# Kernel tuning notes

Measured on AMD Instinct MI355X. Metric: run time of the kernel, lower is better.

The kernel has to match this reference:

```python
import jax, jax.numpy as jnp
import numpy as np
import math

B, S, H = 2, 4096, 768
NH, HD = 12, 64  # num heads, head dim


def setup_inputs() -> dict:
    key = jax.random.key(0)
    ks = jax.random.split(key, 4)
    scale = 1.0 / math.sqrt(H)
    return {
        "hidden_states": jax.random.normal(ks[0], (B, S, H), jnp.float32),
        "attention_mask": jnp.zeros((B, 1, 1, S), jnp.float32),
        "Wq": jax.random.normal(ks[1], (H, H), jnp.float32) * scale,
        "bq": jnp.zeros((H,), jnp.float32),
        "Wk": jax.random.normal(ks[2], (H, H), jnp.float32) * scale,
        "bk": jnp.zeros((H,), jnp.float32),
        "Wv": jax.random.normal(ks[3], (H, H), jnp.float32) * scale,
        "bv": jnp.zeros((H,), jnp.float32),
    }


def reference(hidden_states, attention_mask, Wq, bq, Wk, bk, Wv, bv):
    # Linear projections (torch nn.Linear: x @ W.T + b)
    q = hidden_states @ Wq.T + bq  # [B,S,H]
    k = hidden_states @ Wk.T + bk
    v = hidden_states @ Wv.T + bv
    # split heads -> [B, NH, S, HD]
    def split(x):
        return x.reshape(B, S, NH, HD).transpose(0, 2, 1, 3)
    qh, kh, vh = split(q), split(k), split(v)
    scores = jnp.einsum('bhqd,bhkd->bhqk', qh, kh) / math.sqrt(HD)
    scores = scores + attention_mask  # additive mask, broadcast
    probs = jax.nn.softmax(scores, axis=-1)
    # dropout prob = 0.0 (inference) -> identity
    ctx = jnp.einsum('bhqk,bhkd->bhqd', probs, vh)
    ctx = ctx.transpose(0, 2, 1, 3).reshape(B, S, H)
    return ctx
```

## Files before the change

### kernel.cpp

```cpp
#include <hip/hip_runtime.h>
#include <hip/hip_bf16.h>

typedef float f32x4 __attribute__((ext_vector_type(4)));
typedef short short8 __attribute__((ext_vector_type(8)));

#define LOG2E 1.44269504088896340736f

__device__ __forceinline__ ushort f2bf(float f){
  unsigned u = __builtin_bit_cast(unsigned, f);
  u = (u + 0x7fffu + ((u >> 16) & 1u)) >> 16;
  return (ushort)u;
}

__device__ __forceinline__ float exp2_hw(float x){
  float r; asm("v_exp_f32 %0, %1" : "=v"(r) : "v"(x)); return r;
}

__device__ __forceinline__ uint pack_bf16_rh(float lo, float hi){
  uint ul = __builtin_bit_cast(uint, lo) + 0x8000u;
  uint uh = __builtin_bit_cast(uint, hi) + 0x8000u;
  return __builtin_amdgcn_perm(uh, ul, 0x07060302u);
}

__device__ __forceinline__ float fmax3(float a, float b, float c){
  return fmaxf(fmaxf(a, b), c);
}

__global__ void cvt_kernel(const float* __restrict__ src, ushort* __restrict__ dst, int n4){
  int i = blockIdx.x * 256 + threadIdx.x;
  if (i < n4){
    float4 v = ((const float4*)src)[i];
    ushort4 o; o.x = f2bf(v.x); o.y = f2bf(v.y); o.z = f2bf(v.z); o.w = f2bf(v.w);
    ((ushort4*)dst)[i] = o;
  }
}

__global__ void scale_kernel(const float* __restrict__ src, float* __restrict__ dst,
                             float sc, int n){
  int i = blockIdx.x * 256 + threadIdx.x;
  if (i < n) dst[i] = src[i] * sc;
}

__global__ __launch_bounds__(256) void qkv_gemm(const ushort* __restrict__ Xb,
                                                const ushort* __restrict__ Wb,
                                                const float* __restrict__ bias,
                                                ushort* __restrict__ Out,
                                                float scale){
  __shared__ ushort Xs[128*64];
  __shared__ ushort Ws[128*64];
  const int m0 = blockIdx.x * 128, n0 = blockIdx.y * 128;
  const int tid = threadIdx.x, w = tid >> 6, lane = tid & 63;
  const int r = lane & 15, g = lane >> 4;
  const int wr = (w >> 1) * 64, wc = (w & 1) * 64;
  f32x4 acc[4][4] = {};
  for (int k0 = 0; k0 < 768; k0 += 64){
    #pragma unroll
    for (int p = 0; p < 4; p++){
      int c = tid + 256*p; int row = c >> 3, cir = c & 7;
      uint4 vx = *(const uint4*)(Xb + (size_t)(m0+row)*768 + k0 + cir*8);
      *(uint4*)((char*)Xs + row*128 + ((cir*16) ^ ((row&7)<<4))) = vx;
      uint4 vw = *(const uint4*)(Wb + (size_t)(n0+row)*768 + k0 + cir*8);
      *(uint4*)((char*)Ws + row*128 + ((cir*16) ^ ((row&7)<<4))) = vw;
    }
    __syncthreads();
    #pragma unroll
    for (int ks = 0; ks < 2; ks++){
      short8 af[4], bf[4];
      int bo = ks*64 + g*16;
      #pragma unroll
      for (int i = 0; i < 4; i++){
        int rowa = wr + i*16 + r;
        af[i] = *(const short8*)((char*)Xs + rowa*128 + (bo ^ ((rowa&7)<<4)));
        int rowb = wc + i*16 + r;
        bf[i] = *(const short8*)((char*)Ws + rowb*128 + (bo ^ ((rowb&7)<<4)));
      }
      #pragma unroll
      for (int i = 0; i < 4; i++)
        #pragma unroll
        for (int j = 0; j < 4; j++)
          acc[i][j] = __builtin_amdgcn_mfma_f32_16x16x32_bf16(af[i], bf[j], acc[i][j], 0,0,0);
    }
    __syncthreads();
  }
  #pragma unroll
  for (int i = 0; i < 4; i++){
    #pragma unroll
    for (int j = 0; j < 4; j++){
      int col = n0 + wc + j*16 + r;
      float bv = bias[col];
      int rowb = m0 + wr + i*16 + g*4;
      #pragma unroll
      for (int q = 0; q < 4; q++)
        Out[(size_t)(rowb+q)*768 + col] = f2bf((acc[i][j][q] + bv) * scale);
    }
  }
}

__global__ __launch_bounds__(256) void qkv_gemm_vt(const ushort* __restrict__ Xb,
                                                   const ushort* __restrict__ Wb,
                                                   const float* __restrict__ bias,
                                                   ushort* __restrict__ VtOut){
  __shared__ ushort Xs[128*64];
  __shared__ ushort Ws[128*64];
  const int m0 = blockIdx.x * 128, n0 = blockIdx.y * 128;
  const int tid = threadIdx.x, w = tid >> 6, lane = tid & 63;
  const int r = lane & 15, g = lane >> 4;
  const int wr = (w >> 1) * 64, wc = (w & 1) * 64;
  f32x4 acc[4][4] = {};
  for (int k0 = 0; k0 < 768; k0 += 64){
    #pragma unroll
    for (int p = 0; p < 4; p++){
      int c = tid + 256*p; int row = c >> 3, cir = c & 7;
      uint4 vx = *(const uint4*)(Xb + (size_t)(m0+row)*768 + k0 + cir*8);
      *(uint4*)((char*)Xs + row*128 + ((cir*16) ^ ((row&7)<<4))) = vx;
      uint4 vw = *(const uint4*)(Wb + (size_t)(n0+row)*768 + k0 + cir*8);
      *(uint4*)((char*)Ws + row*128 + ((cir*16) ^ ((row&7)<<4))) = vw;
    }
    __syncthreads();
    #pragma unroll
    for (int ks = 0; ks < 2; ks++){
      short8 af[4], bf[4];
      int bo = ks*64 + g*16;
      #pragma unroll
      for (int i = 0; i < 4; i++){
        int rowa = wr + i*16 + r;
        af[i] = *(const short8*)((char*)Xs + rowa*128 + (bo ^ ((rowa&7)<<4)));
        int rowb = wc + i*16 + r;
        bf[i] = *(const short8*)((char*)Ws + rowb*128 + (bo ^ ((rowb&7)<<4)));
      }
      #pragma unroll
      for (int i = 0; i < 4; i++)
        #pragma unroll
        for (int j = 0; j < 4; j++)
          acc[i][j] = __builtin_amdgcn_mfma_f32_16x16x32_bf16(af[i], bf[j], acc[i][j], 0,0,0);
    }
    __syncthreads();
  }
  #pragma unroll
  for (int i = 0; i < 4; i++){
    #pragma unroll
    for (int j = 0; j < 4; j++){
      int col = n0 + wc + j*16 + r;
      float bv = bias[col];
      int rowb = m0 + wr + i*16 + g*4;
      ushort4 o;
      o.x = f2bf(acc[i][j][0] + bv);
      o.y = f2bf(acc[i][j][1] + bv);
      o.z = f2bf(acc[i][j][2] + bv);
      o.w = f2bf(acc[i][j][3] + bv);
      size_t vrow = (size_t)((rowb >> 12) * 768 + col);
      *(ushort4*)(VtOut + vrow * 4096 + (rowb & 4095)) = o;
    }
  }
}

__global__ __launch_bounds__(256, 3) void flash_attn(const ushort* __restrict__ Qb,
                                                     const ushort* __restrict__ Kb,
                                                     const ushort* __restrict__ Vt,
                                                     const float* __restrict__ maskL,
                                                     float* __restrict__ out){
  __shared__ ushort Ks[64*64];
  __shared__ ushort Vts[64*64];
  __shared__ ushort Ps[4][2048];
  const int tid = threadIdx.x, w = tid >> 6, lane = tid & 63;
  const int r = lane & 15, g = lane >> 4;
  const int swr = (r & 7) << 4;
  const int h = blockIdx.y, b = blockIdx.z;
  const int q0 = blockIdx.x * 128 + w * 32;
  char* Pw = (char*)(Ps[w]);

  short8 bq[2][2];
  #pragma unroll
  for (int grp = 0; grp < 2; grp++){
    const ushort* qp = Qb + (size_t)(b*4096 + q0 + grp*16 + r)*768 + h*64 + g*8;
    bq[grp][0] = *(const short8*)qp;
    bq[grp][1] = *(const short8*)(qp + 32);
  }
  const ushort* Kbase = Kb + (size_t)(b*4096)*768 + h*64;
  const ushort* Vbase = Vt + (size_t)(b*768 + h*64)*4096;

  const int row0 = tid >> 3, cir = tid & 7;
  const int row1 = row0 + 32;

  uint4 kreg0, kreg1, vreg0, vreg1;
  kreg0 = *(const uint4*)(Kbase + (size_t)row0*768 + cir*8);
  kreg1 = *(const uint4*)(Kbase + (size_t)row1*768 + cir*8);
  vreg0 = *(const uint4*)(Vbase + (size_t)row0*4096 + cir*8);
  vreg1 = *(const uint4*)(Vbase + (size_t)row1*4096 + cir*8);

  f32x4 ctx[2][4] = {};
  float mrun[2] = {-1e30f, -1e30f}, lrun[2] = {0.f, 0.f};

  for (int t = 0; t < 64; t++){
    const int kv0 = t * 64;
    *(uint4*)((char*)Ks  + row0*128 + ((cir*16) ^ ((row0&7)<<4))) = kreg0;
    *(uint4*)((char*)Ks  + row1*128 + ((cir*16) ^ ((row1&7)<<4))) = kreg1;
    *(uint4*)((char*)Vts + row0*128 + ((cir*16) ^ ((row0&7)<<4))) = vreg0;
    *(uint4*)((char*)Vts + row1*128 + ((cir*16) ^ ((row1&7)<<4))) = vreg1;
    __syncthreads();
    if (t < 63){
      const int kn = kv0 + 64;
      kreg0 = *(const uint4*)(Kbase + (size_t)(kn+row0)*768 + cir*8);
      kreg1 = *(const uint4*)(Kbase + (size_t)(kn+row1)*768 + cir*8);
      vreg0 = *(const uint4*)(Vbase + (size_t)row0*4096 + kn + cir*8);
      vreg1 = *(const uint4*)(Vbase + (size_t)row1*4096 + kn + cir*8);
    }
    f32x4 s[2][4];
    #pragma unroll
    for (int c = 0; c < 4; c++){
      int row = c*16 + r; int sw = (row&7) << 4;
      const char* base = (const char*)Ks + row*128;
      short8 ak0 = *(const short8*)(base + ((g*16) ^ sw));
      short8 ak1 = *(const short8*)(base + ((64 + g*16) ^ sw));
      #pragma unroll
      for (int grp = 0; grp < 2; grp++){
        f32x4 z = {};
        z = __builtin_amdgcn_mfma_f32_16x16x32_bf16(ak0, bq[grp][0], z, 0,0,0);
        z = __builtin_amdgcn_mfma_f32_16x16x32_bf16(ak1, bq[grp][1], z, 0,0,0);
        s[grp][c] = z;
      }
    }
    #pragma unroll
    for (int c = 0; c < 4; c++){
      float4 mv = *(const float4*)(maskL + b*4096 + kv0 + c*16 + g*4);
      #pragma unroll
      for (int grp = 0; grp < 2; grp++){
        s[grp][c][0] += mv.x; s[grp][c][1] += mv.y;
        s[grp][c][2] += mv.z; s[grp][c][3] += mv.w;
      }
    }
    #pragma unroll
    for (int grp = 0; grp < 2; grp++){
      float ma = fmax3(s[grp][0][0], s[grp][0][1], s[grp][0][2]);
      ma = fmax3(ma, s[grp][0][3], s[grp][1][0]);
      ma = fmax3(ma, s[grp][1][1], s[grp][1][2]);
      float mb = fmax3(s[grp][1][3], s[grp][2][0], s[grp][2][1]);
      mb = fmax3(mb, s[grp][2][2], s[grp][2][3]);
      mb = fmax3(mb, s[grp][3][0], s[grp][3][1]);
      float mt = fmax3(s[grp][3][2], s[grp][3][3], fmaxf(ma, mb));
      mt = fmaxf(mt, __shfl_xor(mt, 16, 64));
      mt = fmaxf(mt, __shfl_xor(mt, 32, 64));
      if (!__all(mt <= mrun[grp] + 11.5415603f)){
        float mnew = fmaxf(mrun[grp], mt);
        float alpha = exp2_hw(mrun[grp] - mnew);
        mrun[grp] = mnew;
        lrun[grp] *= alpha;
        #pragma unroll
        for (int j = 0; j < 4; j++)
          #pragma unroll
          for (int e = 0; e < 4; e++) ctx[grp][j][e] *= alpha;
      }
      float rs = 0.f;
      #pragma unroll
      for (int c = 0; c < 4; c++)
        #pragma unroll
        for (int e = 0; e < 4; e++){
          float pv = exp2_hw(s[grp][c][e] - mrun[grp]); s[grp][c][e] = pv; rs += pv;
        }
      rs += __shfl_xor(rs, 16, 64);
      rs += __shfl_xor(rs, 32, 64);
      lrun[grp] += rs;
      char* Pr = Pw + (grp*16 + r)*128;
      #pragma unroll
      for (int c = 0; c < 4; c++){
        uint2 du;
        du.x = pack_bf16_rh(s[grp][c][0], s[grp][c][1]);
        du.y = pack_bf16_rh(s[grp][c][2], s[grp][c][3]);
        *(uint2*)(Pr + ((c*32 + g*8) ^ swr)) = du;
      }
    }
    short8 bp[2][2];
    #pragma unroll
    for (int grp = 0; grp < 2; grp++){
      const char* Pr = Pw + (grp*16 + r)*128;
      bp[grp][0] = *(const short8*)(Pr + ((g*16) ^ swr));
      bp[grp][1] = *(const short8*)(Pr + ((64 + g*16) ^ swr));
    }
    #pragma unroll
    for (int j = 0; j < 4; j++){
      int row = j*16 + r; int sw = (row&7) << 4;
      const char* base = (const char*)Vts + row*128;
      short8 av0 = *(const short8*)(base + ((g*16) ^ sw));
      short8 av1 = *(const short8*)(base + ((64 + g*16) ^ sw));
      #pragma unroll
      for (int grp = 0; grp < 2; grp++){
        ctx[grp][j] = __builtin_amdgcn_mfma_f32_16x16x32_bf16(av0, bp[grp][0], ctx[grp][j], 0,0,0);
        ctx[grp][j] = __builtin_amdgcn_mfma_f32_16x16x32_bf16(av1, bp[grp][1], ctx[grp][j], 0,0,0);
      }
    }
    __syncthreads();
  }
  #pragma unroll
  for (int grp = 0; grp < 2; grp++){
    float inv = 1.0f / lrun[grp];
    size_t orow = (size_t)(b*4096 + q0 + grp*16 + r) * 768 + h*64;
    #pragma unroll
    for (int j = 0; j < 4; j++){
      float4 o;
      o.x = ctx[grp][j][0] * inv; o.y = ctx[grp][j][1] * inv;
      o.z = ctx[grp][j][2] * inv; o.w = ctx[grp][j][3] * inv;
      *(float4*)(out + orow + j*16 + g*4) = o;
    }
  }
}

extern "C" void kernel_launch(void* const* d_in, const int* in_sizes, int n_in,
                              void* d_out, int out_size, void* d_ws, size_t ws_size,
                              hipStream_t stream){
  const float* hidden = (const float*)d_in[0];
  const float* mask   = (const float*)d_in[1];
  const float* Wq     = (const float*)d_in[2];
  const float* bq     = (const float*)d_in[3];
  const float* Wk     = (const float*)d_in[4];
  const float* bk     = (const float*)d_in[5];
  const float* Wv     = (const float*)d_in[6];
  const float* bv     = (const float*)d_in[7];
  char* ws = (char*)d_ws;
  ushort* Xb    = (ushort*)(ws);
  ushort* Wqb   = (ushort*)(ws + 12582912);
  ushort* Wkb   = (ushort*)(ws + 13762560);
  ushort* Wvb   = (ushort*)(ws + 14942208);
  ushort* Qb    = (ushort*)(ws + 16121856);
  ushort* Kb    = (ushort*)(ws + 28704768);
  ushort* Vtb   = (ushort*)(ws + 41287680);
  float*  maskL = (float*)(ws + 53870592);

  cvt_kernel<<<6144, 256, 0, stream>>>(hidden, Xb, 1572864);
  cvt_kernel<<<576, 256, 0, stream>>>(Wq, Wqb, 147456);
  cvt_kernel<<<576, 256, 0, stream>>>(Wk, Wkb, 147456);
  cvt_kernel<<<576, 256, 0, stream>>>(Wv, Wvb, 147456);
  scale_kernel<<<32, 256, 0, stream>>>(mask, maskL, LOG2E, 8192);

  dim3 gg(64, 6);
  qkv_gemm<<<gg, 256, 0, stream>>>(Xb, Wqb, bq, Qb, 0.125f * LOG2E);
  qkv_gemm<<<gg, 256, 0, stream>>>(Xb, Wkb, bk, Kb, 1.0f);
  qkv_gemm_vt<<<gg, 256, 0, stream>>>(Xb, Wvb, bv, Vtb);

  dim3 ga(32, 12, 2);
  flash_attn<<<ga, 256, 0, stream>>>(Qb, Kb, Vtb, maskL, (float*)d_out);
}
```

Before: 232.9 us.

## Use 32x32x16 MFMA and keep P in registers via permlane32 swap

Rewrites the flash-attention inner loop to use 32x32x16 bf16 MFMA tiles instead of 16x16x32, so each wave owns 32 query rows as one tile with a single running max and sum per lane. The probability matrix is no longer written to and read back from LDS. It is packed to bf16 and rearranged across lane halves with v_permlane32_swap, then fed straight into the PV MFMA. This removes the per-wave P shared buffer and its LDS traffic, and cuts the cross-lane softmax reductions. In exchange it relies on the permlane32 swap instruction and on the larger MFMA's register layout being mapped correctly.

```diff
diff --git a/kernel.cpp b/kernel.cpp
--- a/kernel.cpp
+++ b/kernel.cpp
@@ -2,6 +2,7 @@
 #include <hip/hip_bf16.h>
 
 typedef float f32x4 __attribute__((ext_vector_type(4)));
+typedef float f32x16 __attribute__((ext_vector_type(16)));
 typedef short short8 __attribute__((ext_vector_type(8)));
 
 #define LOG2E 1.44269504088896340736f
@@ -161,20 +162,17 @@
                                                      float* __restrict__ out){
   __shared__ ushort Ks[64*64];
   __shared__ ushort Vts[64*64];
-  __shared__ ushort Ps[4][2048];
   const int tid = threadIdx.x, w = tid >> 6, lane = tid & 63;
-  const int r = lane & 15, g = lane >> 4;
-  const int swr = (r & 7) << 4;
+  const int q = lane & 31, hi = lane >> 5;
+  const int swq = (q & 7) << 4;
   const int h = blockIdx.y, b = blockIdx.z;
   const int q0 = blockIdx.x * 128 + w * 32;
-  char* Pw = (char*)(Ps[w]);
-
-  short8 bq[2][2];
-  #pragma unroll
-  for (int grp = 0; grp < 2; grp++){
-    const ushort* qp = Qb + (size_t)(b*4096 + q0 + grp*16 + r)*768 + h*64 + g*8;
-    bq[grp][0] = *(const short8*)qp;
-    bq[grp][1] = *(const short8*)(qp + 32);
+
+  short8 bq[4];
+  {
+    const ushort* qp = Qb + (size_t)(b*4096 + q0 + q)*768 + h*64 + hi*8;
+    #pragma unroll
+    for (int kd = 0; kd < 4; kd++) bq[kd] = *(const short8*)(qp + 16*kd);
   }
   const ushort* Kbase = Kb + (size_t)(b*4096)*768 + h*64;
   const ushort* Vbase = Vt + (size_t)(b*768 + h*64)*4096;
@@ -188,8 +186,8 @@
   vreg0 = *(const uint4*)(Vbase + (size_t)row0*4096 + cir*8);
   vreg1 = *(const uint4*)(Vbase + (size_t)row1*4096 + cir*8);
 
-  f32x4 ctx[2][4] = {};
-  float mrun[2] = {-1e30f, -1e30f}, lrun[2] = {0.f, 0.f};
+  f32x16 ctx[2] = {};
+  float mrun = -1e30f, lrun = 0.f;
 
   for (int t = 0; t < 64; t++){
     const int kv0 = t * 64;
@@ -205,103 +203,98 @@
       vreg0 = *(const uint4*)(Vbase + (size_t)row0*4096 + kn + cir*8);
       vreg1 = *(const uint4*)(Vbase + (size_t)row1*4096 + kn + cir*8);
     }
-    f32x4 s[2][4];
-    #pragma unroll
-    for (int c = 0; c < 4; c++){
-      int row = c*16 + r; int sw = (row&7) << 4;
-      const char* base = (const char*)Ks + row*128;
-      short8 ak0 = *(const short8*)(base + ((g*16) ^ sw));
-      short8 ak1 = *(const short8*)(base + ((64 + g*16) ^ sw));
-      #pragma unroll
-      for (int grp = 0; grp < 2; grp++){
-        f32x4 z = {};
-        z = __builtin_amdgcn_mfma_f32_16x16x32_bf16(ak0, bq[grp][0], z, 0,0,0);
-        z = __builtin_amdgcn_mfma_f32_16x16x32_bf16(ak1, bq[grp][1], z, 0,0,0);
-        s[grp][c] = z;
-      }
-    }
-    #pragma unroll
-    for (int c = 0; c < 4; c++){
-      float4 mv = *(const float4*)(maskL + b*4096 + kv0 + c*16 + g*4);
-      #pragma unroll
-      for (int grp = 0; grp < 2; grp++){
-        s[grp][c][0] += mv.x; s[grp][c][1] += mv.y;
-        s[grp][c][2] += mv.z; s[grp][c][3] += mv.w;
-      }
-    }
-    #pragma unroll
-    for (int grp = 0; grp < 2; grp++){
-      float ma = fmax3(s[grp][0][0], s[grp][0][1], s[grp][0][2]);
-      ma = fmax3(ma, s[grp][0][3], s[grp][1][0]);
-      ma = fmax3(ma, s[grp][1][1], s[grp][1][2]);
-      float mb = fmax3(s[grp][1][3], s[grp][2][0], s[grp][2][1]);
-      mb = fmax3(mb, s[grp][2][2], s[grp][2][3]);
-      mb = fmax3(mb, s[grp][3][0], s[grp][3][1]);
-      float mt = fmax3(s[grp][3][2], s[grp][3][3], fmaxf(ma, mb));
-      mt = fmaxf(mt, __shfl_xor(mt, 16, 64));
-      mt = fmaxf(mt, __shfl_xor(mt, 32, 64));
-      if (!__all(mt <= mrun[grp] + 11.5415603f)){
-        float mnew = fmaxf(mrun[grp], mt);
-        float alpha = exp2_hw(mrun[grp] - mnew);
-        mrun[grp] = mnew;
-        lrun[grp] *= alpha;
+    f32x16 sc[2];
+    #pragma unroll
+    for (int s = 0; s < 2; s++){
+      f32x16 z = {};
+      #pragma unroll
+      for (int kd = 0; kd < 4; kd++){
+        int row = s*32 + q;
+        short8 ak = *(const short8*)((char*)Ks + row*128 + ((32*kd + 16*hi) ^ swq));
+        z = __builtin_amdgcn_mfma_f32_32x32x16_bf16(ak, bq[kd], z, 0,0,0);
+      }
+      sc[s] = z;
+    }
+    #pragma unroll
+    for (int s = 0; s < 2; s++)
+      #pragma unroll
+      for (int eq = 0; eq < 4; eq++){
+        float4 mv = *(const float4*)(maskL + b*4096 + kv0 + s*32 + eq*8 + hi*4);
+        sc[s][4*eq+0] += mv.x; sc[s][4*eq+1] += mv.y;
+        sc[s][4*eq+2] += mv.z; sc[s][4*eq+3] += mv.w;
+      }
+    float ma = fmax3(sc[0][0], sc[0][1], sc[0][2]);
+    float mb = fmax3(sc[0][3], sc[0][4], sc[0][5]);
+    ma = fmax3(ma, sc[0][6], sc[0][7]);
+    mb = fmax3(mb, sc[0][8], sc[0][9]);
+    ma = fmax3(ma, sc[0][10], sc[0][11]);
+    mb = fmax3(mb, sc[0][12], sc[0][13]);
+    ma = fmax3(ma, sc[0][14], sc[0][15]);
+    #pragma unroll
+    for (int e = 0; e < 15; e += 3) mb = fmax3(mb, sc[1][e], sc[1][e+1]);
+    ma = fmax3(ma, sc[1][2], sc[1][5]);
+    ma = fmax3(ma, sc[1][8], sc[1][11]);
+    ma = fmax3(ma, sc[1][14], sc[1][15]);
+    float mt = fmaxf(ma, mb);
+    mt = fmaxf(mt, __shfl_xor(mt, 32, 64));
+    if (!__all(mt <= mrun + 11.5415603f)){
+      float mnew = fmaxf(mrun, mt);
+      float alpha = exp2_hw(mrun - mnew);
+      mrun = mnew;
+      lrun *= alpha;
+      #pragma unroll
+      for (int s = 0; s < 2; s++)
         #pragma unroll
-        for (int j = 0; j < 4; j++)
-          #pragma unroll
-          for (int e = 0; e < 4; e++) ctx[grp][j][e] *= alpha;
-      }
-      float rs = 0.f;
-      #pragma unroll
-      for (int c = 0; c < 4; c++)
-        #pragma unroll
-        for (int e = 0; e < 4; e++){
-          float pv = exp2_hw(s[grp][c][e] - mrun[grp]); s[grp][c][e] = pv; rs += pv;
-        }
-      rs += __shfl_xor(rs, 16, 64);
-      rs += __shfl_xor(rs, 32, 64);
-      lrun[grp] += rs;
-      char* Pr = Pw + (grp*16 + r)*128;
-      #pragma unroll
-      for (int c = 0; c < 4; c++){
-        uint2 du;
-        du.x = pack_bf16_rh(s[grp][c][0], s[grp][c][1]);
-        du.y = pack_bf16_rh(s[grp][c][2], s[grp][c][3]);
-        *(uint2*)(Pr + ((c*32 + g*8) ^ swr)) = du;
-      }
-    }
-    short8 bp[2][2];
-    #pragma unroll
-    for (int grp = 0; grp < 2; grp++){
-      const char* Pr = Pw + (grp*16 + r)*128;
-      bp[grp][0] = *(const short8*)(Pr + ((g*16) ^ swr));
-      bp[grp][1] = *(const short8*)(Pr + ((64 + g*16) ^ swr));
-    }
-    #pragma unroll
-    for (int j = 0; j < 4; j++){
-      int row = j*16 + r; int sw = (row&7) << 4;
-      const char* base = (const char*)Vts + row*128;
-      short8 av0 = *(const short8*)(base + ((g*16) ^ sw));
-      short8 av1 = *(const short8*)(base + ((64 + g*16) ^ sw));
-      #pragma unroll
-      for (int grp = 0; grp < 2; grp++){
-        ctx[grp][j] = __builtin_amdgcn_mfma_f32_16x16x32_bf16(av0, bp[grp][0], ctx[grp][j], 0,0,0);
-        ctx[grp][j] = __builtin_amdgcn_mfma_f32_16x16x32_bf16(av1, bp[grp][1], ctx[grp][j], 0,0,0);
-      }
-    }
-    __syncthreads();
-  }
+        for (int e = 0; e < 16; e++) ctx[s][e] *= alpha;
+    }
+    float rs = 0.f;
+    #pragma unroll
+    for (int s = 0; s < 2; s++)
+      #pragma unroll
+      for (int e = 0; e < 16; e++){
+        float pv = exp2_hw(sc[s][e] - mrun); sc[s][e] = pv; rs += pv;
+      }
+    rs += __shfl_xor(rs, 32, 64);
+    lrun += rs;
+    short8 bp[4];
+    #pragma unroll
+    for (int s = 0; s < 2; s++){
+      uint pw[8];
+      #pragma unroll
+      for (int u = 0; u < 8; u++)
+        pw[u] = pack_bf16_rh(sc[s][2*u], sc[s][2*u+1]);
+      #pragma unroll
+      for (int u2 = 0; u2 < 2; u2++){
+        uint x0 = pw[4*u2+0], x1 = pw[4*u2+1], x2 = pw[4*u2+2], x3 = pw[4*u2+3];
+        asm("v_permlane32_swap_b32 %0, %1" : "+v"(x0), "+v"(x2));
+        asm("v_permlane32_swap_b32 %0, %1" : "+v"(x1), "+v"(x3));
+        union { uint u[4]; short8 v; } bb;
+        bb.u[0] = x0; bb.u[1] = x1; bb.u[2] = x2; bb.u[3] = x3;
+        bp[2*s + u2] = bb.v;
+      }
+    }
+    #pragma unroll
+    for (int sd = 0; sd < 2; sd++){
+      int row = sd*32 + q;
+      #pragma unroll
+      for (int kk = 0; kk < 4; kk++){
+        short8 av = *(const short8*)((char*)Vts + row*128 + ((32*kk + 16*hi) ^ swq));
+        ctx[sd] = __builtin_amdgcn_mfma_f32_32x32x16_bf16(av, bp[kk], ctx[sd], 0,0,0);
+      }
+    }
+    __syncthreads();
+  }
+  float inv = 1.0f / lrun;
+  size_t orow = (size_t)(b*4096 + q0 + q) * 768 + h*64;
   #pragma unroll
-  for (int grp = 0; grp < 2; grp++){
-    float inv = 1.0f / lrun[grp];
-    size_t orow = (size_t)(b*4096 + q0 + grp*16 + r) * 768 + h*64;
-    #pragma unroll
-    for (int j = 0; j < 4; j++){
+  for (int sd = 0; sd < 2; sd++)
+    #pragma unroll
+    for (int eq = 0; eq < 4; eq++){
       float4 o;
-      o.x = ctx[grp][j][0] * inv; o.y = ctx[grp][j][1] * inv;
-      o.z = ctx[grp][j][2] * inv; o.w = ctx[grp][j][3] * inv;
-      *(float4*)(out + orow + j*16 + g*4) = o;
-    }
-  }
+      o.x = ctx[sd][4*eq+0] * inv; o.y = ctx[sd][4*eq+1] * inv;
+      o.z = ctx[sd][4*eq+2] * inv; o.w = ctx[sd][4*eq+3] * inv;
+      *(float4*)(out + orow + sd*32 + eq*8 + hi*4) = o;
+    }
 }
 
 extern "C" void kernel_launch(void* const* d_in, const int* in_sizes, int n_in,
```

Measured after the change: 240.6 us. 3.3% more time.
